# Kernel optimization log

Hardware: AMD Instinct MI355X
Metric: run time of the kernel (lower is better)

## Reference

```python
import jax, jax.numpy as jnp
import numpy as np

D = 768        # d_model
H = 12         # num_heads
HD = D // H    # head dim = 64
LAT = 256      # latent_dim
B = 16
S = 8192
ROPE_BASE = 10000.0


def get_alibi_slopes(n):
    # standard ALiBi geometric slopes for power-of-two-ish head counts
    start = 2.0 ** (-8.0 / n)
    return np.array([start ** (i + 1) for i in range(n)], dtype=np.float32)


def apply_rope(x, pos):
    # x: [B, L, H, HD], pos: [L] float positions
    half = HD // 2
    inv_freq = 1.0 / (ROPE_BASE ** (jnp.arange(0, half, dtype=jnp.float32) / half))
    ang = pos[:, None] * inv_freq                      # [L, half]
    cos = jnp.cos(ang)[None, :, None, :]               # [1, L, 1, half]
    sin = jnp.sin(ang)[None, :, None, :]
    x1, x2 = x[..., :half], x[..., half:]
    return jnp.concatenate([x1 * cos - x2 * sin, x1 * sin + x2 * cos], axis=-1)


def setup_inputs() -> dict:
    key = jax.random.key(0)
    ks = jax.random.split(key, 13)
    s = 1.0 / np.sqrt(D)
    return {
        "x": jax.random.normal(ks[0], (B, S, D), dtype=jnp.float32),
        "pool_token": jax.random.normal(ks[1], (1, 1, D), dtype=jnp.float32),
        "Wq": jax.random.normal(ks[2], (D, D), dtype=jnp.float32) * s,
        "bq": jnp.zeros((D,), dtype=jnp.float32),
        "Wk": jax.random.normal(ks[3], (D, D), dtype=jnp.float32) * s,
        "bk": jnp.zeros((D,), dtype=jnp.float32),
        "Wv": jax.random.normal(ks[4], (D, D), dtype=jnp.float32) * s,
        "bv": jnp.zeros((D,), dtype=jnp.float32),
        "Wo": jax.random.normal(ks[5], (D, D), dtype=jnp.float32) * s,
        "bo": jnp.zeros((D,), dtype=jnp.float32),
        "Wl": jax.random.normal(ks[6], (LAT, D), dtype=jnp.float32) * s,
        "bl": jnp.zeros((LAT,), dtype=jnp.float32),
    }


def reference(x, pool_token, Wq, bq, Wk, bk, Wv, bv, Wo, bo, Wl, bl):
    b = x.shape[0]
    memory = jnp.broadcast_to(pool_token, (b, 1, D))           # learned pooled query

    q = (memory @ Wq.T + bq).reshape(b, 1, H, HD)
    k = (x @ Wk.T + bk).reshape(b, S, H, HD)
    v = (x @ Wv.T + bv).reshape(b, S, H, HD)

    # RoPE: query sits at position 0, keys at positions 0..S-1
    q = apply_rope(q, jnp.zeros((1,), dtype=jnp.float32))
    k = apply_rope(k, jnp.arange(S, dtype=jnp.float32))

    scores = jnp.einsum("bqhd,bkhd->bhqk", q, k) / jnp.sqrt(jnp.float32(HD))  # [B,H,1,S]

    # ALiBi: linear penalty proportional to distance from the query (pos 0)
    slopes = jnp.asarray(get_alibi_slopes(H))                  # [H]
    bias = -slopes[:, None] * jnp.arange(S, dtype=jnp.float32)[None, :]       # [H,S]
    scores = scores + bias[None, :, None, :]

    attn = jax.nn.softmax(scores, axis=-1)                     # [B,H,1,S]
    out = jnp.einsum("bhqk,bkhd->bqhd", attn, v).reshape(b, 1, D)
    pooled = out @ Wo.T + bo                                   # [B,1,D]
    return pooled[:, 0] @ Wl.T + bl                            # [B,LAT]
```

## Files before the change

### kernel.cpp

```cpp
#include <hip/hip_runtime.h>

constexpr int DIM = 768;
constexpr int NH  = 12;
constexpr int HDm = 64;
constexpr int HALF = 32;
constexpr int LATm = 256;
constexpr int NB  = 16;
constexpr int SEQ = 8192;
constexpr int NPRIME = NH * DIM;
constexpr int PSP = 32;
constexpr int PSR = SEQ / PSP;

typedef short bf16x8 __attribute__((ext_vector_type(8)));
typedef float f32x4  __attribute__((ext_vector_type(4)));
using u16 = unsigned short;

__device__ __forceinline__ u16 f2b(float f) {
    unsigned int u = __float_as_uint(f);
    u += 0x7FFFu + ((u >> 16) & 1u);
    return (u16)(u >> 16);
}

__device__ __forceinline__ void gload_lds16(const void* g, void* l) {
    __builtin_amdgcn_global_load_lds(
        (const __attribute__((address_space(1))) unsigned int*)g,
        (__attribute__((address_space(3))) unsigned int*)l, 16, 0, 0);
}

__global__ __launch_bounds__(256) void k_mv(const float* __restrict__ Wb,
        const float* __restrict__ bias, const float* __restrict__ vin,
        float* __restrict__ vout,
        int rows, int batch, int in_bstride, int out_bstride, int headslice) {
    int w = threadIdx.x >> 6, lane = threadIdx.x & 63;
    int gw = blockIdx.x * 4 + w;
    if (gw >= rows * batch) return;
    int b = gw / rows, row = gw - b * rows;
    const float* vi = vin + (size_t)b * in_bstride + (headslice ? (row >> 6) * DIM : 0);
    const float* wr = Wb + (size_t)row * DIM;
    float acc = 0.f;
    #pragma unroll
    for (int c = 0; c < DIM / 64; ++c)
        acc += wr[c * 64 + lane] * vi[c * 64 + lane];
    #pragma unroll
    for (int off = 32; off > 0; off >>= 1) acc += __shfl_xor(acc, off, 64);
    if (lane == 0) vout[(size_t)b * out_bstride + row] = acc + bias[row];
}

__global__ void k_uw(const float* __restrict__ q, const float* __restrict__ Wk,
                     u16* __restrict__ UWpT) {
    int tid = blockIdx.x * 256 + threadIdx.x;
    int np = tid >> 6, c = tid & 63;
    int h = np / DIM, d = np - h * DIM;
    int j = c & 31;
    float q1 = q[h * HDm + j], q2 = q[h * HDm + HALF + j];
    float wa = Wk[(size_t)(h * HDm + j) * DIM + d];
    float wb = Wk[(size_t)(h * HDm + HALF + j) * DIM + d];
    float v = (c < HALF) ? (q1 * wa + q2 * wb) : (q2 * wa - q1 * wb);
    UWpT[(size_t)np * 64 + c] = f2b(v * 0.125f);
}

__global__ void k_T(u16* __restrict__ T) {
    int tid = blockIdx.x * 256 + threadIdx.x;
    int s = tid >> 6, c = tid & 63;
    int j = c & 31;
    float f = expf(-(float)j * (9.210340372f / 32.f));
    float ang = (float)s * f;
    float v = (c < HALF) ? cosf(ang) : sinf(ang);
    T[tid] = f2b(v);
}

__global__ void k_eb(const float* __restrict__ q, const float* __restrict__ bk,
                     float* __restrict__ Ebias) {
    int tid = blockIdx.x * 256 + threadIdx.x;
    if (tid >= SEQ * NH) return;
    int s = tid / NH, h = tid - s * NH;
    float acc = 0.f;
    for (int j = 0; j < HALF; ++j) {
        float f = expf(-(float)j * (9.210340372f / 32.f));
        float sv, cv; sincosf((float)s * f, &sv, &cv);
        float b1 = bk[h * HDm + j], b2 = bk[h * HDm + HALF + j];
        float q1 = q[h * HDm + j], q2 = q[h * HDm + HALF + j];
        acc += cv * (q1 * b1 + q2 * b2) + sv * (q2 * b1 - q1 * b2);
    }
    Ebias[tid] = acc * 0.125f;
}

__global__ void __launch_bounds__(256) k_E(const u16* __restrict__ T,
        const u16* __restrict__ UWpT, u16* __restrict__ E, int s0) {
    __shared__ u16 et[4 * 64 * 72];
    int lane = threadIdx.x & 63, wid = threadIdx.x >> 6;
    int m0 = blockIdx.y * 128 + (wid >> 1) * 64;
    int n0 = blockIdx.x * 128 + (wid & 1) * 64;
    int l15 = lane & 15, quad = lane >> 4;
    f32x4 acc[4][4] = {};
    #pragma unroll
    for (int kq = 0; kq < 2; ++kq) {
        int kb = kq * 32 + quad * 8;
        bf16x8 a[4], b[4];
        #pragma unroll
        for (int i = 0; i < 4; ++i)
            a[i] = *(const bf16x8*)(T + (size_t)(s0 + m0 + i * 16 + l15) * 64 + kb);
        #pragma unroll
        for (int i = 0; i < 4; ++i)
            b[i] = *(const bf16x8*)(UWpT + (size_t)(n0 + i * 16 + l15) * 64 + kb);
        #pragma unroll
        for (int mi = 0; mi < 4; ++mi)
            #pragma unroll
            for (int ni = 0; ni < 4; ++ni)
                acc[mi][ni] = __builtin_amdgcn_mfma_f32_16x16x32_bf16(a[mi], b[ni], acc[mi][ni], 0, 0, 0);
    }
    u16* ep = et + wid * (64 * 72);
    #pragma unroll
    for (int mi = 0; mi < 4; ++mi)
        #pragma unroll
        for (int ni = 0; ni < 4; ++ni) {
            int col_l = ni * 16 + l15;
            #pragma unroll
            for (int r = 0; r < 4; ++r) {
                int row_l = mi * 16 + quad * 4 + r;
                ep[row_l * 72 + col_l] = f2b(acc[mi][ni][r]);
            }
        }
    #pragma unroll
    for (int it = 0; it < 8; ++it) {
        int row_l = it * 8 + (lane >> 3);
        int cols  = (lane & 7) * 8;
        bf16x8 v = *(const bf16x8*)&ep[row_l * 72 + cols];
        *(bf16x8*)(E + (size_t)(m0 + row_l) * NPRIME + n0 + cols) = v;
    }
}

__global__ void __launch_bounds__(256) k_sc(const float* __restrict__ x,
        const u16* __restrict__ E, const float* __restrict__ Ebias,
        float* __restrict__ scores, int s0) {
    __shared__ float xt[16 * 772];
    int t = threadIdx.x, lane = t & 63, w = t >> 6;
    int sl = blockIdx.x;
    int s  = s0 + sl;
    int l15 = lane & 15, quad = lane >> 4;

    const u16* eb = E + (size_t)sl * NPRIME + (size_t)l15 * DIM + w * 6 * 32 + quad * 8;
    bf16x8 bv[6];
    #pragma unroll
    for (int i = 0; i < 6; ++i) bv[i] = *(const bf16x8*)(eb + i * 32);

    #pragma unroll
    for (int i = 0; i < 12; ++i) {
        int idx = w * 12 + i;
        int tt = idx >> 4, b = idx & 15;
        const char* g = (const char*)x + ((size_t)b * SEQ + s) * (DIM * 4) + tt * 1024 + (size_t)lane * 16;
        char* l = (char*)xt + b * 3088 + tt * 1024;
        gload_lds16(g, l);
    }
    asm volatile("s_waitcnt vmcnt(0)" ::: "memory");
    __syncthreads();

    f32x4 acc = {};
    #pragma unroll
    for (int i = 0; i < 6; ++i) {
        int kc = w * 6 + i;
        const float* xr = xt + l15 * 772 + kc * 32 + quad * 8;
        float4 fa = *(const float4*)xr;
        float4 fb = *(const float4*)(xr + 4);
        bf16x8 av;
        av[0] = (short)f2b(fa.x); av[1] = (short)f2b(fa.y);
        av[2] = (short)f2b(fa.z); av[3] = (short)f2b(fa.w);
        av[4] = (short)f2b(fb.x); av[5] = (short)f2b(fb.y);
        av[6] = (short)f2b(fb.z); av[7] = (short)f2b(fb.w);
        acc = __builtin_amdgcn_mfma_f32_16x16x32_bf16(av, bv[i], acc, 0, 0, 0);
    }
    __syncthreads();
    f32x4* red = (f32x4*)xt;
    red[w * 64 + lane] = acc;
    __syncthreads();
    if (t < NB * NH) {
        int b = t / NH, h = t - b * NH;
        int lr = (b >> 2) * 16 + h, r = b & 3;
        float v = red[0 * 64 + lr][r] + red[1 * 64 + lr][r]
                + red[2 * 64 + lr][r] + red[3 * 64 + lr][r];
        float bias = Ebias[s * NH + h] - exp2f(-8.f * (h + 1) / 12.f) * (float)s;
        scores[((size_t)b * NH + h) * SEQ + s] = v + bias;
    }
}

__global__ void __launch_bounds__(1024) k_sm(float* __restrict__ scores) {
    __shared__ float red[1024];
    float* row = scores + (size_t)blockIdx.x * SEQ;
    int t = threadIdx.x;
    float m = -1e30f;
    for (int i = t; i < SEQ; i += 1024) m = fmaxf(m, row[i]);
    red[t] = m; __syncthreads();
    for (int o = 512; o > 0; o >>= 1) { if (t < o) red[t] = fmaxf(red[t], red[t + o]); __syncthreads(); }
    m = red[0]; __syncthreads();
    float sum = 0.f;
    for (int i = t; i < SEQ; i += 1024) sum += expf(row[i] - m);
    red[t] = sum; __syncthreads();
    for (int o = 512; o > 0; o >>= 1) { if (t < o) red[t] += red[t + o]; __syncthreads(); }
    float inv = 1.f / red[0];
    for (int i = t; i < SEQ; i += 1024) row[i] = expf(row[i] - m) * inv;
}

__global__ void __launch_bounds__(256) k_pool(const float* __restrict__ x,
        const float* __restrict__ attn, float* __restrict__ part) {
    __shared__ float attn_s[12 * 256];
    __shared__ float xbuf[2 * 16 * 256];
    int bx = blockIdx.x;
    int sp = bx / 48, rem = bx - sp * 48, b = rem / 3, dc = rem - (rem / 3) * 3;
    int t = threadIdx.x, lane = t & 63, w = t >> 6;

    for (int i = t; i < 12 * 256; i += 256)
        attn_s[i] = attn[((size_t)b * NH + (i >> 8)) * SEQ + sp * PSR + (i & 255)];

    auto stage = [&](int buf, int tt) {
        #pragma unroll
        for (int jj = 0; jj < 4; ++jj) {
            int r = w * 4 + jj;
            const char* g = (const char*)x
                + (((size_t)b * SEQ + sp * PSR + tt * 16 + r) * DIM + dc * 256) * 4
                + (size_t)lane * 16;
            char* l = (char*)xbuf + buf * 16384 + r * 1024;
            gload_lds16(g, l);
        }
    };

    f32x4 acc[12] = {};
    stage(0, 0);
    asm volatile("s_waitcnt vmcnt(0)" ::: "memory");
    __syncthreads();
    for (int tt = 0; tt < 16; ++tt) {
        int cur = tt & 1;
        if (tt < 15) stage(cur ^ 1, tt + 1);
        const float* xb = xbuf + cur * 4096;
        #pragma unroll
        for (int j = 0; j < 4; ++j) {
            int r = w * 4 + j;
            float4 xv = *(const float4*)(xb + r * 256 + lane * 4);
            int si = tt * 16 + r;
            #pragma unroll
            for (int h = 0; h < 12; ++h) {
                float a = attn_s[h * 256 + si];
                acc[h][0] += a * xv.x; acc[h][1] += a * xv.y;
                acc[h][2] += a * xv.z; acc[h][3] += a * xv.w;
            }
        }
        asm volatile("s_waitcnt vmcnt(0)" ::: "memory");
        __syncthreads();
    }
    float* red = xbuf;
    #pragma unroll
    for (int half = 0; half < 2; ++half) {
        __syncthreads();
        #pragma unroll
        for (int hh = 0; hh < 6; ++hh)
            *(f32x4*)(red + ((w * 64 + lane) * 6 + hh) * 4) = acc[half * 6 + hh];
        __syncthreads();
        for (int i = t; i < 6 * 64; i += 256) {
            int hh = i >> 6, dt = i & 63;
            f32x4 v = {};
            #pragma unroll
            for (int ww = 0; ww < 4; ++ww) {
                f32x4 u = *(const f32x4*)(red + ((ww * 64 + dt) * 6 + hh) * 4);
                v[0] += u[0]; v[1] += u[1]; v[2] += u[2]; v[3] += u[3];
            }
            *(f32x4*)(part + ((size_t)(sp * NB + b) * NH + half * 6 + hh) * DIM
                      + dc * 256 + dt * 4) = v;
        }
    }
}

__global__ void k_red(const float* __restrict__ part, float* __restrict__ pooled) {
    int i = blockIdx.x * 256 + threadIdx.x;
    if (i < NB * NH * DIM) {
        float s = 0.f;
        for (int sp = 0; sp < PSP; ++sp) s += part[(size_t)sp * (NB * NH * DIM) + i];
        pooled[i] = s;
    }
}

extern "C" void kernel_launch(void* const* d_in, const int* in_sizes, int n_in,
                              void* d_out, int out_size, void* d_ws, size_t ws_size,
                              hipStream_t stream) {
    (void)in_sizes; (void)n_in; (void)out_size;
    const float* x    = (const float*)d_in[0];
    const float* pool = (const float*)d_in[1];
    const float* Wq   = (const float*)d_in[2];
    const float* bq   = (const float*)d_in[3];
    const float* Wk   = (const float*)d_in[4];
    const float* bk   = (const float*)d_in[5];
    const float* Wv   = (const float*)d_in[6];
    const float* bv   = (const float*)d_in[7];
    const float* Wo   = (const float*)d_in[8];
    const float* bo   = (const float*)d_in[9];
    const float* Wl   = (const float*)d_in[10];
    const float* bl   = (const float*)d_in[11];

    char* w = (char*)d_ws;
    auto alloc = [&](size_t bytes) { char* p = w; w += (bytes + 255) & ~(size_t)255; return p; };
    float* q_f    = (float*)alloc(DIM * 4);
    u16*   UWpT   = (u16*)alloc((size_t)NPRIME * 64 * 2);
    u16*   Tt     = (u16*)alloc((size_t)SEQ * 64 * 2);
    float* Ebias  = (float*)alloc((size_t)SEQ * NH * 4);
    float* scores = (float*)alloc((size_t)NB * NH * SEQ * 4);
    float* part   = (float*)alloc((size_t)PSP * NB * NH * DIM * 4);
    float* pooled = (float*)alloc((size_t)NB * NH * DIM * 4);
    float* o_buf  = (float*)alloc((size_t)NB * DIM * 4);
    float* p_buf  = (float*)alloc((size_t)NB * DIM * 4);

    size_t fixed_used = (size_t)(w - (char*)d_ws);
    size_t margin = 65536;
    size_t avail = (ws_size > fixed_used + margin) ? (ws_size - fixed_used - margin) : 0;
    size_t rows = avail / ((size_t)NPRIME * 2);
    int chunk = (rows >= (size_t)SEQ) ? SEQ : (int)(rows & ~(size_t)127);
    if (chunk < 128) chunk = 128;
    u16* E = (u16*)alloc((size_t)chunk * NPRIME * 2 + 8192);

    hipLaunchKernelGGL(k_mv, dim3(192), dim3(256), 0, stream,
                       Wq, bq, pool, q_f, DIM, 1, 0, DIM, 0);
    hipLaunchKernelGGL(k_uw, dim3(NPRIME * 64 / 256), dim3(256), 0, stream, q_f, Wk, UWpT);
    hipLaunchKernelGGL(k_T, dim3(SEQ * 64 / 256), dim3(256), 0, stream, Tt);
    hipLaunchKernelGGL(k_eb, dim3((SEQ * NH + 255) / 256), dim3(256), 0, stream, q_f, bk, Ebias);
    for (int s0 = 0; s0 < SEQ; s0 += chunk) {
        int cur = (SEQ - s0 < chunk) ? (SEQ - s0) : chunk;
        hipLaunchKernelGGL(k_E, dim3(NPRIME / 128, cur / 128), dim3(256), 0, stream,
                           Tt, UWpT, E, s0);
        hipLaunchKernelGGL(k_sc, dim3(cur), dim3(256), 0, stream,
                           x, E, Ebias, scores, s0);
    }
    hipLaunchKernelGGL(k_sm, dim3(NB * NH), dim3(1024), 0, stream, scores);
    hipLaunchKernelGGL(k_pool, dim3(PSP * NB * 3), dim3(256), 0, stream, x, scores, part);
    hipLaunchKernelGGL(k_red, dim3((NB * NH * DIM + 255) / 256), dim3(256), 0, stream, part, pooled);
    hipLaunchKernelGGL(k_mv, dim3(NB * DIM / 4), dim3(256), 0, stream,
                       Wv, bv, pooled, o_buf, DIM, NB, NH * DIM, DIM, 1);
    hipLaunchKernelGGL(k_mv, dim3(NB * DIM / 4), dim3(256), 0, stream,
                       Wo, bo, o_buf, p_buf, DIM, NB, DIM, DIM, 0);
    hipLaunchKernelGGL(k_mv, dim3(NB * LATm / 4), dim3(256), 0, stream,
                       Wl, bl, p_buf, (float*)d_out, LATm, NB, DIM, LATm, 0);
}
```

Measured before the change: 749.0 us.

## Fuse rope-key matrix generation with score computation, register-cache softmax

Replaces the two-kernel path, which wrote a large per-position bf16 E matrix (SEQ x 9216) to global memory and read it back, with one fused k_score kernel. For each 16-position block, k_score builds E tiles in LDS with MFMA from Tt and UWpT. It then multiplies them against double-buffered, XOR-swizzled x tiles loaded straight into LDS. This removes the global round-trip of E and the chunking loop. The softmax kernel now keeps its 8 values per thread in registers, so exp is computed once and the row is read once. The cost is more UWpT reloads per block and extra barriers inside the fused loop.

```diff
diff --git a/kernel.cpp b/kernel.cpp
--- a/kernel.cpp
+++ b/kernel.cpp
@@ -12,6 +12,7 @@
 constexpr int PSR = SEQ / PSP;
 
 typedef short bf16x8 __attribute__((ext_vector_type(8)));
+typedef short bf16x4 __attribute__((ext_vector_type(4)));
 typedef float f32x4  __attribute__((ext_vector_type(4)));
 using u16 = unsigned short;
 
@@ -85,101 +86,106 @@
     Ebias[tid] = acc * 0.125f;
 }
 
-__global__ void __launch_bounds__(256) k_E(const u16* __restrict__ T,
-        const u16* __restrict__ UWpT, u16* __restrict__ E, int s0) {
-    __shared__ u16 et[4 * 64 * 72];
-    int lane = threadIdx.x & 63, wid = threadIdx.x >> 6;
-    int m0 = blockIdx.y * 128 + (wid >> 1) * 64;
-    int n0 = blockIdx.x * 128 + (wid & 1) * 64;
+constexpr int SBLK = 16;
+constexpr int DCH  = 32;
+constexpr int NDC  = DIM / DCH;
+constexpr int ES_S = 880;
+constexpr int ES_H = 72;
+constexpr int XBUF = 16 * SBLK * 128;
+
+__global__ void __launch_bounds__(256) k_score(const float* __restrict__ x,
+        const u16* __restrict__ Tt, const u16* __restrict__ UWpT,
+        const float* __restrict__ Ebias, float* __restrict__ scores) {
+    __shared__ char lds[2 * XBUF + 14464];
+    char* es = lds + 2 * XBUF;
+    int t = threadIdx.x, lane = t & 63, w = t >> 6;
+    int S0 = blockIdx.x * SBLK;
     int l15 = lane & 15, quad = lane >> 4;
-    f32x4 acc[4][4] = {};
-    #pragma unroll
-    for (int kq = 0; kq < 2; ++kq) {
-        int kb = kq * 32 + quad * 8;
-        bf16x8 a[4], b[4];
-        #pragma unroll
-        for (int i = 0; i < 4; ++i)
-            a[i] = *(const bf16x8*)(T + (size_t)(s0 + m0 + i * 16 + l15) * 64 + kb);
-        #pragma unroll
-        for (int i = 0; i < 4; ++i)
-            b[i] = *(const bf16x8*)(UWpT + (size_t)(n0 + i * 16 + l15) * 64 + kb);
-        #pragma unroll
-        for (int mi = 0; mi < 4; ++mi)
+
+    bf16x8 tb[2];
+    #pragma unroll
+    for (int kq = 0; kq < 2; ++kq)
+        tb[kq] = *(const bf16x8*)(Tt + (size_t)(S0 + l15) * 64 + kq * 32 + quad * 8);
+
+    auto stage = [&](int buf, int dc2) {
+        #pragma unroll
+        for (int i = 0; i < 8; ++i) {
+            int j = w * 8 + i;
+            int row = j * 8 + (lane >> 3);
+            int b = row >> 4, sl = row & 15;
+            const char* g = (const char*)x
+                + ((size_t)(b * SEQ + S0 + sl) * DIM + dc2 * DCH) * 4
+                + (((lane & 7) ^ (b & 7)) * 16);
+            gload_lds16(g, lds + buf * XBUF + j * 1024);
+        }
+    };
+
+    stage(0, 0);
+    f32x4 sacc[4] = {};
+
+    for (int dc = 0; dc < NDC; ++dc) {
+        int cur = dc & 1;
+        bf16x8 ua[6][2];
+        #pragma unroll
+        for (int mt = 0; mt < 6; ++mt) {
+            int npl = (w * 6 + mt) * 16 + l15;
+            int np = (npl >> 5) * DIM + dc * DCH + (npl & 31);
             #pragma unroll
-            for (int ni = 0; ni < 4; ++ni)
-                acc[mi][ni] = __builtin_amdgcn_mfma_f32_16x16x32_bf16(a[mi], b[ni], acc[mi][ni], 0, 0, 0);
-    }
-    u16* ep = et + wid * (64 * 72);
-    #pragma unroll
-    for (int mi = 0; mi < 4; ++mi)
-        #pragma unroll
-        for (int ni = 0; ni < 4; ++ni) {
-            int col_l = ni * 16 + l15;
+            for (int kq = 0; kq < 2; ++kq)
+                ua[mt][kq] = *(const bf16x8*)(UWpT + (size_t)np * 64 + kq * 32 + quad * 8);
+        }
+        if (dc < NDC - 1) stage(cur ^ 1, dc + 1);
+        #pragma unroll
+        for (int mt = 0; mt < 6; ++mt) {
+            f32x4 ea = {};
+            ea = __builtin_amdgcn_mfma_f32_16x16x32_bf16(ua[mt][0], tb[0], ea, 0, 0, 0);
+            ea = __builtin_amdgcn_mfma_f32_16x16x32_bf16(ua[mt][1], tb[1], ea, 0, 0, 0);
+            int npl = (w * 6 + mt) * 16 + quad * 4;
+            int h = npl >> 5, dd0 = npl & 31;
+            bf16x4 pv;
+            pv[0] = (short)f2b(ea[0]); pv[1] = (short)f2b(ea[1]);
+            pv[2] = (short)f2b(ea[2]); pv[3] = (short)f2b(ea[3]);
+            *(bf16x4*)(es + l15 * ES_S + h * ES_H + dd0 * 2) = pv;
+        }
+        asm volatile("s_waitcnt lgkmcnt(0)" ::: "memory");
+        __builtin_amdgcn_s_barrier();
+        const char* xb = lds + cur * XBUF;
+        #pragma unroll
+        for (int si = 0; si < 4; ++si) {
+            int sloc = w * 4 + si;
+            const char* xrow = xb + (l15 * 16 + sloc) * 128;
+            float4 fa = *(const float4*)(xrow + (((2 * quad)     ^ (l15 & 7)) * 16));
+            float4 fb = *(const float4*)(xrow + (((2 * quad + 1) ^ (l15 & 7)) * 16));
+            bf16x8 av;
+            av[0] = (short)f2b(fa.x); av[1] = (short)f2b(fa.y);
+            av[2] = (short)f2b(fa.z); av[3] = (short)f2b(fa.w);
+            av[4] = (short)f2b(fb.x); av[5] = (short)f2b(fb.y);
+            av[6] = (short)f2b(fb.z); av[7] = (short)f2b(fb.w);
+            const char* ep = es + sloc * ES_S + l15 * ES_H + quad * 16;
+            bf16x4 b0 = *(const bf16x4*)ep;
+            bf16x4 b1 = *(const bf16x4*)(ep + 8);
+            bf16x8 bv;
+            bv[0] = b0[0]; bv[1] = b0[1]; bv[2] = b0[2]; bv[3] = b0[3];
+            bv[4] = b1[0]; bv[5] = b1[1]; bv[6] = b1[2]; bv[7] = b1[3];
+            sacc[si] = __builtin_amdgcn_mfma_f32_16x16x32_bf16(av, bv, sacc[si], 0, 0, 0);
+        }
+        asm volatile("s_waitcnt lgkmcnt(0)" ::: "memory");
+        __builtin_amdgcn_s_barrier();
+    }
+
+    int h = l15;
+    if (h < NH) {
+        float slope = exp2f(-8.f * (h + 1) / 12.f);
+        #pragma unroll
+        for (int si = 0; si < 4; ++si) {
+            int s = S0 + w * 4 + si;
+            float bias = Ebias[s * NH + h] - slope * (float)s;
             #pragma unroll
             for (int r = 0; r < 4; ++r) {
-                int row_l = mi * 16 + quad * 4 + r;
-                ep[row_l * 72 + col_l] = f2b(acc[mi][ni][r]);
+                int b = quad * 4 + r;
+                scores[((size_t)b * NH + h) * SEQ + s] = sacc[si][r] + bias;
             }
         }
-    #pragma unroll
-    for (int it = 0; it < 8; ++it) {
-        int row_l = it * 8 + (lane >> 3);
-        int cols  = (lane & 7) * 8;
-        bf16x8 v = *(const bf16x8*)&ep[row_l * 72 + cols];
-        *(bf16x8*)(E + (size_t)(m0 + row_l) * NPRIME + n0 + cols) = v;
-    }
-}
-
-__global__ void __launch_bounds__(256) k_sc(const float* __restrict__ x,
-        const u16* __restrict__ E, const float* __restrict__ Ebias,
-        float* __restrict__ scores, int s0) {
-    __shared__ float xt[16 * 772];
-    int t = threadIdx.x, lane = t & 63, w = t >> 6;
-    int sl = blockIdx.x;
-    int s  = s0 + sl;
-    int l15 = lane & 15, quad = lane >> 4;
-
-    const u16* eb = E + (size_t)sl * NPRIME + (size_t)l15 * DIM + w * 6 * 32 + quad * 8;
-    bf16x8 bv[6];
-    #pragma unroll
-    for (int i = 0; i < 6; ++i) bv[i] = *(const bf16x8*)(eb + i * 32);
-
-    #pragma unroll
-    for (int i = 0; i < 12; ++i) {
-        int idx = w * 12 + i;
-        int tt = idx >> 4, b = idx & 15;
-        const char* g = (const char*)x + ((size_t)b * SEQ + s) * (DIM * 4) + tt * 1024 + (size_t)lane * 16;
-        char* l = (char*)xt + b * 3088 + tt * 1024;
-        gload_lds16(g, l);
-    }
-    asm volatile("s_waitcnt vmcnt(0)" ::: "memory");
-    __syncthreads();
-
-    f32x4 acc = {};
-    #pragma unroll
-    for (int i = 0; i < 6; ++i) {
-        int kc = w * 6 + i;
-        const float* xr = xt + l15 * 772 + kc * 32 + quad * 8;
-        float4 fa = *(const float4*)xr;
-        float4 fb = *(const float4*)(xr + 4);
-        bf16x8 av;
-        av[0] = (short)f2b(fa.x); av[1] = (short)f2b(fa.y);
-        av[2] = (short)f2b(fa.z); av[3] = (short)f2b(fa.w);
-        av[4] = (short)f2b(fb.x); av[5] = (short)f2b(fb.y);
-        av[6] = (short)f2b(fb.z); av[7] = (short)f2b(fb.w);
-        acc = __builtin_amdgcn_mfma_f32_16x16x32_bf16(av, bv[i], acc, 0, 0, 0);
-    }
-    __syncthreads();
-    f32x4* red = (f32x4*)xt;
-    red[w * 64 + lane] = acc;
-    __syncthreads();
-    if (t < NB * NH) {
-        int b = t / NH, h = t - b * NH;
-        int lr = (b >> 2) * 16 + h, r = b & 3;
-        float v = red[0 * 64 + lr][r] + red[1 * 64 + lr][r]
-                + red[2 * 64 + lr][r] + red[3 * 64 + lr][r];
-        float bias = Ebias[s * NH + h] - exp2f(-8.f * (h + 1) / 12.f) * (float)s;
-        scores[((size_t)b * NH + h) * SEQ + s] = v + bias;
     }
 }
 
@@ -187,17 +193,21 @@
     __shared__ float red[1024];
     float* row = scores + (size_t)blockIdx.x * SEQ;
     int t = threadIdx.x;
+    float v[8];
     float m = -1e30f;
-    for (int i = t; i < SEQ; i += 1024) m = fmaxf(m, row[i]);
+    #pragma unroll
+    for (int i = 0; i < 8; ++i) { v[i] = row[t + i * 1024]; m = fmaxf(m, v[i]); }
     red[t] = m; __syncthreads();
     for (int o = 512; o > 0; o >>= 1) { if (t < o) red[t] = fmaxf(red[t], red[t + o]); __syncthreads(); }
     m = red[0]; __syncthreads();
     float sum = 0.f;
-    for (int i = t; i < SEQ; i += 1024) sum += expf(row[i] - m);
+    #pragma unroll
+    for (int i = 0; i < 8; ++i) { v[i] = expf(v[i] - m); sum += v[i]; }
     red[t] = sum; __syncthreads();
     for (int o = 512; o > 0; o >>= 1) { if (t < o) red[t] += red[t + o]; __syncthreads(); }
     float inv = 1.f / red[0];
-    for (int i = t; i < SEQ; i += 1024) row[i] = expf(row[i] - m) * inv;
+    #pragma unroll
+    for (int i = 0; i < 8; ++i) row[t + i * 1024] = v[i] * inv;
 }
 
 __global__ void __launch_bounds__(256) k_pool(const float* __restrict__ x,
@@ -280,7 +290,7 @@
 extern "C" void kernel_launch(void* const* d_in, const int* in_sizes, int n_in,
                               void* d_out, int out_size, void* d_ws, size_t ws_size,
                               hipStream_t stream) {
-    (void)in_sizes; (void)n_in; (void)out_size;
+    (void)in_sizes; (void)n_in; (void)out_size; (void)ws_size;
     const float* x    = (const float*)d_in[0];
     const float* pool = (const float*)d_in[1];
     const float* Wq   = (const float*)d_in[2];
@@ -306,26 +316,13 @@
     float* o_buf  = (float*)alloc((size_t)NB * DIM * 4);
     float* p_buf  = (float*)alloc((size_t)NB * DIM * 4);
 
-    size_t fixed_used = (size_t)(w - (char*)d_ws);
-    size_t margin = 65536;
-    size_t avail = (ws_size > fixed_used + margin) ? (ws_size - fixed_used - margin) : 0;
-    size_t rows = avail / ((size_t)NPRIME * 2);
-    int chunk = (rows >= (size_t)SEQ) ? SEQ : (int)(rows & ~(size_t)127);
-    if (chunk < 128) chunk = 128;
-    u16* E = (u16*)alloc((size_t)chunk * NPRIME * 2 + 8192);
-
     hipLaunchKernelGGL(k_mv, dim3(192), dim3(256), 0, stream,
                        Wq, bq, pool, q_f, DIM, 1, 0, DIM, 0);
     hipLaunchKernelGGL(k_uw, dim3(NPRIME * 64 / 256), dim3(256), 0, stream, q_f, Wk, UWpT);
     hipLaunchKernelGGL(k_T, dim3(SEQ * 64 / 256), dim3(256), 0, stream, Tt);
     hipLaunchKernelGGL(k_eb, dim3((SEQ * NH + 255) / 256), dim3(256), 0, stream, q_f, bk, Ebias);
-    for (int s0 = 0; s0 < SEQ; s0 += chunk) {
-        int cur = (SEQ - s0 < chunk) ? (SEQ - s0) : chunk;
-        hipLaunchKernelGGL(k_E, dim3(NPRIME / 128, cur / 128), dim3(256), 0, stream,
-                           Tt, UWpT, E, s0);
-        hipLaunchKernelGGL(k_sc, dim3(cur), dim3(256), 0, stream,
-                           x, E, Ebias, scores, s0);
-    }
+    hipLaunchKernelGGL(k_score, dim3(SEQ / SBLK), dim3(256), 0, stream,
+                       x, Tt, UWpT, Ebias, scores);
     hipLaunchKernelGGL(k_sm, dim3(NB * NH), dim3(1024), 0, stream, scores);
     hipLaunchKernelGGL(k_pool, dim3(PSP * NB * 3), dim3(256), 0, stream, x, scores, part);
     hipLaunchKernelGGL(k_red, dim3((NB * NH * DIM + 255) / 256), dim3(256), 0, stream, part, pooled);
```

Result: faster. 715.0 us (-4.5%).
